# Performance work log

Measured on AMD Instinct MI355X. Metric: run time of the kernel, lower is better.

Reference implementation:

```python
import jax, jax.numpy as jnp
import numpy as np

N_NODES = 50000
N_EDGES = 800000
IN_DIM = 128
HID_DIM = 128
OUT_DIM = 64


def setup_inputs() -> dict:
    key = jax.random.key(0)
    ks = jax.random.split(key, 6)
    x = jax.random.normal(ks[0], (N_NODES, IN_DIM), dtype=jnp.float32)
    row = jax.random.randint(ks[1], (N_EDGES,), 0, N_NODES, dtype=jnp.int32)
    col = jax.random.randint(ks[2], (N_EDGES,), 0, N_NODES, dtype=jnp.int32)
    vals = jax.random.uniform(ks[3], (N_EDGES,), dtype=jnp.float32)
    # Xavier-uniform init as in nn.init.xavier_uniform_
    lim1 = float(np.sqrt(6.0 / (IN_DIM + HID_DIM)))
    lim2 = float(np.sqrt(6.0 / (HID_DIM + OUT_DIM)))
    W1 = jax.random.uniform(ks[4], (IN_DIM, HID_DIM), minval=-lim1, maxval=lim1, dtype=jnp.float32)
    W2 = jax.random.uniform(ks[5], (HID_DIM, OUT_DIM), minval=-lim2, maxval=lim2, dtype=jnp.float32)
    return {"x": x, "row": row, "col": col, "vals": vals, "W1": W1, "W2": W2}


def _spmm(row, col, vals, x):
    # out[i] = sum_{e: row[e]==i} vals[e] * x[col[e]]   (sparse adj @ x)
    msgs = vals[:, None] * x[col]  # [E, D] gathered edge messages
    return jax.ops.segment_sum(msgs, row, num_segments=N_NODES)


def reference(x, row, col, vals, W1, W2):
    # GCN layer 1: adj.mm(x) -> linear -> relu  (dropout = identity in eval)
    h = jax.nn.relu(_spmm(row, col, vals, x) @ W1)
    # GCN layer 2: adj.mm(h) -> linear (no activation)
    out = _spmm(row, col, vals, h) @ W2
    return out
```

## Files before the change

### kernel.cpp

```cpp
#include <hip/hip_runtime.h>
#include <stdint.h>

#define N_NODES 50000
#define N_EDGES 800000
#define IN_DIM 128
#define HID_DIM 128
#define OUT_DIM 64

#define ELL_CAP 64
#define XCD_GROUPS 8
#define ROWS_PER_XCD (N_NODES / XCD_GROUPS)
#define SCAT_BLOCKS_PER_XCD 256
#define SCAT_BLOCKS (SCAT_BLOCKS_PER_XCD * XCD_GROUPS)

#define INIT_BLOCKS 3300

typedef short bf16x8 __attribute__((ext_vector_type(8)));
typedef float f32x4  __attribute__((ext_vector_type(4)));

__device__ __forceinline__ uint32_t pack_bf16x2(float a, float b) {
    uint32_t ba = __float_as_uint(a), bb = __float_as_uint(b);
    ba = (ba + 0x7fffu + ((ba >> 16) & 1u)) >> 16;
    bb = (bb + 0x7fffu + ((bb >> 16) & 1u)) & 0xffff0000u;
    return ba | bb;
}

__device__ __forceinline__ unsigned short f2bf(float f) {
    uint32_t u = __float_as_uint(f);
    return (unsigned short)((u + 0x7fffu + ((u >> 16) & 1u)) >> 16);
}

__device__ __forceinline__ uint8_t f2fp8(float f) {
    uint32_t u = __float_as_uint(f);
    uint32_t s = (u >> 24) & 0x80u;
    uint32_t au = u & 0x7fffffffu;
    uint32_t r = au + 0x7FFFFu + ((au >> 20) & 1u);
    int e = (int)((r >> 23) & 0xffu) - 120;
    uint32_t m = (r >> 20) & 7u;
    uint32_t out;
    if (e <= 0) out = 0u;
    else if (e >= 16) out = 0x7Eu;
    else out = ((uint32_t)e << 3) | m;
    return (uint8_t)(s | out);
}

__device__ __forceinline__ uint32_t pack_edge(int col, float v) {
    uint32_t fb = __float_as_uint(v);
    fb = (fb + 0x7fffu + ((fb >> 16) & 1u)) & 0xffff0000u;
    return fb | (uint32_t)col;
}


__global__ __launch_bounds__(256) void init_all(int* __restrict__ counts,
                                                const float* __restrict__ W1,
                                                const float* __restrict__ W2,
                                                unsigned short* __restrict__ wt1,
                                                unsigned short* __restrict__ wt2,
                                                const int* __restrict__ col,
                                                const float* __restrict__ vals,
                                                uint32_t* __restrict__ epk) {
    int i = blockIdx.x * 256 + threadIdx.x;
    if (i < N_NODES) counts[i] = 0;
    int j = i - N_NODES;
    if (j >= 0 && j < 128 * 128) {
        int n = j >> 7, k = j & 127;
        wt1[j] = f2bf(W1[k * 128 + n]);
    }
    int l = j - 128 * 128;
    if (l >= 0 && l < 64 * 128) {
        int n = l >> 7, k = l & 127;
        wt2[l] = f2bf(W2[k * 64 + n]);
    }
    if (i < N_EDGES) epk[i] = pack_edge(col[i], vals[i]);
}


__global__ __launch_bounds__(256) void scatter_ell(const int* __restrict__ row,
                                                   const uint32_t* __restrict__ epk,
                                                   int* __restrict__ counts,
                                                   uint32_t* __restrict__ ell) {
    const int xcd = blockIdx.x & (XCD_GROUPS - 1);
    const int blk = blockIdx.x >> 3;
    const int rlo = xcd * ROWS_PER_XCD;
    int e = blk * 256 + threadIdx.x;
    const int stride = SCAT_BLOCKS_PER_XCD * 256;
    for (; e < N_EDGES; e += stride) {
        int r = row[e];
        if ((unsigned)(r - rlo) < (unsigned)ROWS_PER_XCD) {
            int p = atomicAdd(&counts[r], 1);
            if (p < ELL_CAP)
                ell[((size_t)r << 6) + p] = epk[e];
        }
    }
}


__global__ __launch_bounds__(256) void gemm_mfma1(const float* __restrict__ x,
                                                  const unsigned short* __restrict__ wt1,
                                                  uint8_t* __restrict__ t1f8) {
    const int tid = threadIdx.x;
    const int wid = tid >> 6, lane = tid & 63;
    const int l15 = lane & 15, lk = lane >> 4;
    const int n0 = blockIdx.y * 64;

    bf16x8 bfrag[4][4];
#pragma unroll
    for (int t = 0; t < 4; ++t) {
        const unsigned short* wp = wt1 + (size_t)(n0 + t * 16 + l15) * 128 + lk * 8;
#pragma unroll
        for (int s = 0; s < 4; ++s)
            bfrag[t][s] = *reinterpret_cast<const bf16x8*>(wp + s * 32);
    }

    for (int mt = blockIdx.x * 4 + wid; mt < 3125; mt += 784) {
        const int arow = mt * 16 + l15;
        bf16x8 afrag[4];
        const float* ap = x + (size_t)arow * 128 + lk * 8;
#pragma unroll
        for (int s = 0; s < 4; ++s) {
            float4 p0 = *reinterpret_cast<const float4*>(ap + s * 32);
            float4 p1 = *reinterpret_cast<const float4*>(ap + s * 32 + 4);
            bf16x8 f;
            f[0] = (short)f2bf(p0.x); f[1] = (short)f2bf(p0.y);
            f[2] = (short)f2bf(p0.z); f[3] = (short)f2bf(p0.w);
            f[4] = (short)f2bf(p1.x); f[5] = (short)f2bf(p1.y);
            f[6] = (short)f2bf(p1.z); f[7] = (short)f2bf(p1.w);
            afrag[s] = f;
        }

        f32x4 acc[4] = {{0.f,0.f,0.f,0.f},{0.f,0.f,0.f,0.f},{0.f,0.f,0.f,0.f},{0.f,0.f,0.f,0.f}};
#pragma unroll
        for (int s = 0; s < 4; ++s)
#pragma unroll
            for (int t = 0; t < 4; ++t)
                acc[t] = __builtin_amdgcn_mfma_f32_16x16x32_bf16(afrag[s], bfrag[t][s], acc[t], 0, 0, 0);

#pragma unroll
        for (int t = 0; t < 4; ++t)
#pragma unroll
            for (int q = 0; q < 4; ++q) {
                int r = mt * 16 + lk * 4 + q;
                t1f8[(size_t)r * 128 + n0 + t * 16 + l15] = f2fp8(acc[t][q]);
            }
    }
}


__global__ __launch_bounds__(256) void gemm_mfma2(const uint32_t* __restrict__ Apk,
                                                  const unsigned short* __restrict__ Wt,
                                                  unsigned short* __restrict__ outb) {
    const int tid = threadIdx.x;
    const int wid = tid >> 6, lane = tid & 63;
    const int l15 = lane & 15, lk = lane >> 4;

    bf16x8 bfrag[4][4];
#pragma unroll
    for (int t = 0; t < 4; ++t) {
        const unsigned short* wp = Wt + (size_t)(t * 16 + l15) * 128 + lk * 8;
#pragma unroll
        for (int s = 0; s < 4; ++s)
            bfrag[t][s] = *reinterpret_cast<const bf16x8*>(wp + s * 32);
    }

    for (int mt = blockIdx.x * 4 + wid; mt < 3125; mt += 784) {
        const int arow = mt * 16 + l15;
        bf16x8 afrag[4];
        const uint32_t* ap = Apk + (size_t)arow * 64 + lk * 4;
#pragma unroll
        for (int s = 0; s < 4; ++s)
            afrag[s] = *reinterpret_cast<const bf16x8*>(ap + s * 16);

        f32x4 acc[4] = {{0.f,0.f,0.f,0.f},{0.f,0.f,0.f,0.f},{0.f,0.f,0.f,0.f},{0.f,0.f,0.f,0.f}};
#pragma unroll
        for (int s = 0; s < 4; ++s)
#pragma unroll
            for (int t = 0; t < 4; ++t)
                acc[t] = __builtin_amdgcn_mfma_f32_16x16x32_bf16(afrag[s], bfrag[t][s], acc[t], 0, 0, 0);

#pragma unroll
        for (int t = 0; t < 4; ++t)
#pragma unroll
            for (int q = 0; q < 4; ++q) {
                int r = mt * 16 + lk * 4 + q;
                outb[(size_t)r * 64 + t * 16 + l15] = f2bf(acc[t][q]);
            }
    }
}


template<bool RELU>
__global__ __launch_bounds__(256) void spmm_fp8_128(const int* __restrict__ counts,
                                                    const uint32_t* __restrict__ ell,
                                                    const uint8_t* __restrict__ x8,
                                                    uint32_t* __restrict__ outp) {
    __shared__ float lut[256];
    {
        int b = threadIdx.x;
        uint32_t ee = (b >> 3) & 15u, mm = b & 7u;
        float f = (ee == 0) ? ldexpf((float)mm, -9) : ldexpf((float)(8 + mm), (int)ee - 10);
        lut[b] = (b & 0x80) ? -f : f;
    }
    __syncthreads();

    const int wid = threadIdx.x >> 6;
    const int lane = threadIdx.x & 63;
    const int r = blockIdx.x * 4 + wid;
    if (r >= N_NODES) return;
    const int start = r << 6;
    int cnt = counts[r]; if (cnt > ELL_CAP) cnt = ELL_CAP;
    const int end = start + cnt;
    const uint8_t* xb = x8 + lane * 2;

    float alo[4] = {0.f, 0.f, 0.f, 0.f};
    float ahi[4] = {0.f, 0.f, 0.f, 0.f};
    int e = start;
    for (; e + 7 < end; e += 8) {
        uint32_t c0 = ell[e],     c1 = ell[e + 1], c2 = ell[e + 2], c3 = ell[e + 3];
        uint32_t c4 = ell[e + 4], c5 = ell[e + 5], c6 = ell[e + 6], c7 = ell[e + 7];
        unsigned short u0 = *reinterpret_cast<const unsigned short*>(xb + (size_t)(c0 & 0xffffu) * 128);
        unsigned short u1 = *reinterpret_cast<const unsigned short*>(xb + (size_t)(c1 & 0xffffu) * 128);
        unsigned short u2 = *reinterpret_cast<const unsigned short*>(xb + (size_t)(c2 & 0xffffu) * 128);
        unsigned short u3 = *reinterpret_cast<const unsigned short*>(xb + (size_t)(c3 & 0xffffu) * 128);
        unsigned short u4 = *reinterpret_cast<const unsigned short*>(xb + (size_t)(c4 & 0xffffu) * 128);
        unsigned short u5 = *reinterpret_cast<const unsigned short*>(xb + (size_t)(c5 & 0xffffu) * 128);
        unsigned short u6 = *reinterpret_cast<const unsigned short*>(xb + (size_t)(c6 & 0xffffu) * 128);
        unsigned short u7 = *reinterpret_cast<const unsigned short*>(xb + (size_t)(c7 & 0xffffu) * 128);
        float v0 = __uint_as_float(c0 & 0xffff0000u), v1 = __uint_as_float(c1 & 0xffff0000u);
        float v2 = __uint_as_float(c2 & 0xffff0000u), v3 = __uint_as_float(c3 & 0xffff0000u);
        float v4 = __uint_as_float(c4 & 0xffff0000u), v5 = __uint_as_float(c5 & 0xffff0000u);
        float v6 = __uint_as_float(c6 & 0xffff0000u), v7 = __uint_as_float(c7 & 0xffff0000u);
        alo[0] = fmaf(v0, lut[u0 & 0xff], alo[0]); ahi[0] = fmaf(v0, lut[u0 >> 8], ahi[0]);
        alo[1] = fmaf(v1, lut[u1 & 0xff], alo[1]); ahi[1] = fmaf(v1, lut[u1 >> 8], ahi[1]);
        alo[2] = fmaf(v2, lut[u2 & 0xff], alo[2]); ahi[2] = fmaf(v2, lut[u2 >> 8], ahi[2]);
        alo[3] = fmaf(v3, lut[u3 & 0xff], alo[3]); ahi[3] = fmaf(v3, lut[u3 >> 8], ahi[3]);
        alo[0] = fmaf(v4, lut[u4 & 0xff], alo[0]); ahi[0] = fmaf(v4, lut[u4 >> 8], ahi[0]);
        alo[1] = fmaf(v5, lut[u5 & 0xff], alo[1]); ahi[1] = fmaf(v5, lut[u5 >> 8], ahi[1]);
        alo[2] = fmaf(v6, lut[u6 & 0xff], alo[2]); ahi[2] = fmaf(v6, lut[u6 >> 8], ahi[2]);
        alo[3] = fmaf(v7, lut[u7 & 0xff], alo[3]); ahi[3] = fmaf(v7, lut[u7 >> 8], ahi[3]);
    }
    if (e + 3 < end) {
        uint32_t c0 = ell[e], c1 = ell[e + 1], c2 = ell[e + 2], c3 = ell[e + 3];
        unsigned short u0 = *reinterpret_cast<const unsigned short*>(xb + (size_t)(c0 & 0xffffu) * 128);
        unsigned short u1 = *reinterpret_cast<const unsigned short*>(xb + (size_t)(c1 & 0xffffu) * 128);
        unsigned short u2 = *reinterpret_cast<const unsigned short*>(xb + (size_t)(c2 & 0xffffu) * 128);
        unsigned short u3 = *reinterpret_cast<const unsigned short*>(xb + (size_t)(c3 & 0xffffu) * 128);
        float v0 = __uint_as_float(c0 & 0xffff0000u), v1 = __uint_as_float(c1 & 0xffff0000u);
        float v2 = __uint_as_float(c2 & 0xffff0000u), v3 = __uint_as_float(c3 & 0xffff0000u);
        alo[0] = fmaf(v0, lut[u0 & 0xff], alo[0]); ahi[0] = fmaf(v0, lut[u0 >> 8], ahi[0]);
        alo[1] = fmaf(v1, lut[u1 & 0xff], alo[1]); ahi[1] = fmaf(v1, lut[u1 >> 8], ahi[1]);
        alo[2] = fmaf(v2, lut[u2 & 0xff], alo[2]); ahi[2] = fmaf(v2, lut[u2 >> 8], ahi[2]);
        alo[3] = fmaf(v3, lut[u3 & 0xff], alo[3]); ahi[3] = fmaf(v3, lut[u3 >> 8], ahi[3]);
        e += 4;
    }
    for (; e < end; ++e) {
        uint32_t c0 = ell[e];
        float v0 = __uint_as_float(c0 & 0xffff0000u);
        unsigned short u0 = *reinterpret_cast<const unsigned short*>(xb + (size_t)(c0 & 0xffffu) * 128);
        alo[0] = fmaf(v0, lut[u0 & 0xff], alo[0]); ahi[0] = fmaf(v0, lut[u0 >> 8], ahi[0]);
    }
    float rlo = (alo[0] + alo[1]) + (alo[2] + alo[3]);
    float rhi = (ahi[0] + ahi[1]) + (ahi[2] + ahi[3]);
    if (RELU) { rlo = fmaxf(rlo, 0.f); rhi = fmaxf(rhi, 0.f); }
    outp[(size_t)r * 64 + lane] = pack_bf16x2(rlo, rhi);
}


__global__ __launch_bounds__(256) void spmm_bf16_64(const int* __restrict__ counts,
                                                    const uint32_t* __restrict__ ell,
                                                    const uint32_t* __restrict__ xp,
                                                    float* __restrict__ out) {
    const int wid = threadIdx.x >> 6;
    const int lane = threadIdx.x & 63;
    const int r = blockIdx.x * 4 + wid;
    if (r >= N_NODES) return;
    const int start = r << 6;
    int cnt = counts[r]; if (cnt > ELL_CAP) cnt = ELL_CAP;
    const int end = start + cnt;
    const int j = lane & 31;
    const int half = lane >> 5;
    const uint32_t* xb = xp + j;

    float alo[4] = {0.f, 0.f, 0.f, 0.f};
    float ahi[4] = {0.f, 0.f, 0.f, 0.f};
    int e = start + half;
    for (; e + 6 < end; e += 8) {
        uint32_t c0 = ell[e], c1 = ell[e + 2], c2 = ell[e + 4], c3 = ell[e + 6];
        uint32_t u0 = xb[(size_t)(c0 & 0xffffu) * 32];
        uint32_t u1 = xb[(size_t)(c1 & 0xffffu) * 32];
        uint32_t u2 = xb[(size_t)(c2 & 0xffffu) * 32];
        uint32_t u3 = xb[(size_t)(c3 & 0xffffu) * 32];
        float v0 = __uint_as_float(c0 & 0xffff0000u), v1 = __uint_as_float(c1 & 0xffff0000u);
        float v2 = __uint_as_float(c2 & 0xffff0000u), v3 = __uint_as_float(c3 & 0xffff0000u);
        alo[0] = fmaf(v0, __uint_as_float(u0 << 16), alo[0]);
        ahi[0] = fmaf(v0, __uint_as_float(u0 & 0xffff0000u), ahi[0]);
        alo[1] = fmaf(v1, __uint_as_float(u1 << 16), alo[1]);
        ahi[1] = fmaf(v1, __uint_as_float(u1 & 0xffff0000u), ahi[1]);
        alo[2] = fmaf(v2, __uint_as_float(u2 << 16), alo[2]);
        ahi[2] = fmaf(v2, __uint_as_float(u2 & 0xffff0000u), ahi[2]);
        alo[3] = fmaf(v3, __uint_as_float(u3 << 16), alo[3]);
        ahi[3] = fmaf(v3, __uint_as_float(u3 & 0xffff0000u), ahi[3]);
    }
    for (; e < end; e += 2) {
        uint32_t c0 = ell[e];
        float v = __uint_as_float(c0 & 0xffff0000u);
        uint32_t u = xb[(size_t)(c0 & 0xffffu) * 32];
        alo[0] = fmaf(v, __uint_as_float(u << 16), alo[0]);
        ahi[0] = fmaf(v, __uint_as_float(u & 0xffff0000u), ahi[0]);
    }
    float alo_s = (alo[0] + alo[1]) + (alo[2] + alo[3]);
    float ahi_s = (ahi[0] + ahi[1]) + (ahi[2] + ahi[3]);
    alo_s += __shfl_xor(alo_s, 32);
    ahi_s += __shfl_xor(ahi_s, 32);
    if (half == 0) {
        float2 res = {alo_s, ahi_s};
        *reinterpret_cast<float2*>(out + (size_t)r * 64 + j * 2) = res;
    }
}


extern "C" void kernel_launch(void* const* d_in, const int* in_sizes, int n_in,
                              void* d_out, int out_size, void* d_ws, size_t ws_size,
                              hipStream_t stream) {
    const float* x    = (const float*)d_in[0];
    const int*   row  = (const int*)  d_in[1];
    const int*   col  = (const int*)  d_in[2];
    const float* vals = (const float*)d_in[3];
    const float* W1   = (const float*)d_in[4];
    const float* W2   = (const float*)d_in[5];
    float* out = (float*)d_out;

    char* ws = (char*)d_ws;
    auto align = [](size_t v) { return (v + 255) & ~(size_t)255; };
    int*      counts  = (int*)ws;              ws += align(sizeof(int) * N_NODES);
    uint32_t* epk     = (uint32_t*)ws;         ws += align(sizeof(uint32_t) * N_EDGES);
    uint32_t* ell     = (uint32_t*)ws;         ws += align(sizeof(uint32_t) * N_NODES * ELL_CAP);
    uint8_t*  t1f8    = (uint8_t*)ws;          ws += align(sizeof(uint8_t) * N_NODES * 128);
    uint32_t* hpk     = (uint32_t*)ws;         ws += align(sizeof(uint32_t) * N_NODES * 64);
    uint32_t* tpk     = (uint32_t*)ws;         ws += align(sizeof(uint32_t) * N_NODES * 32);
    unsigned short* wt1 = (unsigned short*)ws; ws += align(sizeof(short) * 128 * 128);
    unsigned short* wt2 = (unsigned short*)ws; ws += align(sizeof(short) * 64 * 128);

    init_all<<<INIT_BLOCKS, 256, 0, stream>>>(counts, W1, W2, wt1, wt2, col, vals, epk);

    scatter_ell<<<SCAT_BLOCKS, 256, 0, stream>>>(row, epk, counts, ell);

    gemm_mfma1<<<dim3(196, 2), 256, 0, stream>>>(x, wt1, t1f8);
    spmm_fp8_128<true><<<(N_NODES + 3) / 4, 256, 0, stream>>>(counts, ell, t1f8, hpk);

    gemm_mfma2<<<196, 256, 0, stream>>>(hpk, wt2, (unsigned short*)tpk);
    spmm_bf16_64<<<(N_NODES + 3) / 4, 256, 0, stream>>>(counts, ell, tpk, out);
}
```

Measured before the change: 126.6 us.

## Split SpMM feature matrices into column halves to shrink gather working set

The GEMMs now write their outputs as two separate half-width column panels, and each SpMM runs as two launches, one per panel. Each launch gathers from a table half the size (3.2 MB fp8 or 3.2 MB bf16), so the randomly indexed rows are more likely to stay in L2 or the last-level cache. In exchange, the ELL index stream and counts are read twice, there are two extra kernel launches, and each gathered row segment is narrower (64 or 32 bytes), which may waste cache-line bandwidth.

```diff
diff --git a/kernel.cpp b/kernel.cpp
--- a/kernel.cpp
+++ b/kernel.cpp
@@ -97,11 +97,13 @@
 
 __global__ __launch_bounds__(256) void gemm_mfma1(const float* __restrict__ x,
                                                   const unsigned short* __restrict__ wt1,
-                                                  uint8_t* __restrict__ t1f8) {
+                                                  uint8_t* __restrict__ t1a,
+                                                  uint8_t* __restrict__ t1b) {
     const int tid = threadIdx.x;
     const int wid = tid >> 6, lane = tid & 63;
     const int l15 = lane & 15, lk = lane >> 4;
     const int n0 = blockIdx.y * 64;
+    uint8_t* dst = (blockIdx.y == 0) ? t1a : t1b;
 
     bf16x8 bfrag[4][4];
 #pragma unroll
@@ -140,7 +142,7 @@
 #pragma unroll
             for (int q = 0; q < 4; ++q) {
                 int r = mt * 16 + lk * 4 + q;
-                t1f8[(size_t)r * 128 + n0 + t * 16 + l15] = f2fp8(acc[t][q]);
+                dst[(size_t)r * 64 + t * 16 + l15] = f2fp8(acc[t][q]);
             }
     }
 }
@@ -148,7 +150,8 @@
 
 __global__ __launch_bounds__(256) void gemm_mfma2(const uint32_t* __restrict__ Apk,
                                                   const unsigned short* __restrict__ Wt,
-                                                  unsigned short* __restrict__ outb) {
+                                                  unsigned short* __restrict__ t2a,
+                                                  unsigned short* __restrict__ t2b) {
     const int tid = threadIdx.x;
     const int wid = tid >> 6, lane = tid & 63;
     const int l15 = lane & 15, lk = lane >> 4;
@@ -182,17 +185,19 @@
 #pragma unroll
             for (int q = 0; q < 4; ++q) {
                 int r = mt * 16 + lk * 4 + q;
-                outb[(size_t)r * 64 + t * 16 + l15] = f2bf(acc[t][q]);
+                int d = t * 16 + l15;
+                unsigned short* dst = (d < 32) ? t2a : t2b;
+                dst[(size_t)r * 32 + (d & 31)] = f2bf(acc[t][q]);
             }
     }
 }
 
 
-template<bool RELU>
-__global__ __launch_bounds__(256) void spmm_fp8_128(const int* __restrict__ counts,
-                                                    const uint32_t* __restrict__ ell,
-                                                    const uint8_t* __restrict__ x8,
-                                                    uint32_t* __restrict__ outp) {
+__global__ __launch_bounds__(256) void spmm_half_fp8(const int* __restrict__ counts,
+                                                     const uint32_t* __restrict__ ell,
+                                                     const uint8_t* __restrict__ x8h,
+                                                     uint32_t* __restrict__ outp,
+                                                     int word_off) {
     __shared__ float lut[256];
     {
         int b = threadIdx.x;
@@ -202,73 +207,6 @@
     }
     __syncthreads();
 
-    const int wid = threadIdx.x >> 6;
-    const int lane = threadIdx.x & 63;
-    const int r = blockIdx.x * 4 + wid;
-    if (r >= N_NODES) return;
-    const int start = r << 6;
-    int cnt = counts[r]; if (cnt > ELL_CAP) cnt = ELL_CAP;
-    const int end = start + cnt;
-    const uint8_t* xb = x8 + lane * 2;
-
-    float alo[4] = {0.f, 0.f, 0.f, 0.f};
-    float ahi[4] = {0.f, 0.f, 0.f, 0.f};
-    int e = start;
-    for (; e + 7 < end; e += 8) {
-        uint32_t c0 = ell[e],     c1 = ell[e + 1], c2 = ell[e + 2], c3 = ell[e + 3];
-        uint32_t c4 = ell[e + 4], c5 = ell[e + 5], c6 = ell[e + 6], c7 = ell[e + 7];
-        unsigned short u0 = *reinterpret_cast<const unsigned short*>(xb + (size_t)(c0 & 0xffffu) * 128);
-        unsigned short u1 = *reinterpret_cast<const unsigned short*>(xb + (size_t)(c1 & 0xffffu) * 128);
-        unsigned short u2 = *reinterpret_cast<const unsigned short*>(xb + (size_t)(c2 & 0xffffu) * 128);
-        unsigned short u3 = *reinterpret_cast<const unsigned short*>(xb + (size_t)(c3 & 0xffffu) * 128);
-        unsigned short u4 = *reinterpret_cast<const unsigned short*>(xb + (size_t)(c4 & 0xffffu) * 128);
-        unsigned short u5 = *reinterpret_cast<const unsigned short*>(xb + (size_t)(c5 & 0xffffu) * 128);
-        unsigned short u6 = *reinterpret_cast<const unsigned short*>(xb + (size_t)(c6 & 0xffffu) * 128);
-        unsigned short u7 = *reinterpret_cast<const unsigned short*>(xb + (size_t)(c7 & 0xffffu) * 128);
-        float v0 = __uint_as_float(c0 & 0xffff0000u), v1 = __uint_as_float(c1 & 0xffff0000u);
-        float v2 = __uint_as_float(c2 & 0xffff0000u), v3 = __uint_as_float(c3 & 0xffff0000u);
-        float v4 = __uint_as_float(c4 & 0xffff0000u), v5 = __uint_as_float(c5 & 0xffff0000u);
-        float v6 = __uint_as_float(c6 & 0xffff0000u), v7 = __uint_as_float(c7 & 0xffff0000u);
-        alo[0] = fmaf(v0, lut[u0 & 0xff], alo[0]); ahi[0] = fmaf(v0, lut[u0 >> 8], ahi[0]);
-        alo[1] = fmaf(v1, lut[u1 & 0xff], alo[1]); ahi[1] = fmaf(v1, lut[u1 >> 8], ahi[1]);
-        alo[2] = fmaf(v2, lut[u2 & 0xff], alo[2]); ahi[2] = fmaf(v2, lut[u2 >> 8], ahi[2]);
-        alo[3] = fmaf(v3, lut[u3 & 0xff], alo[3]); ahi[3] = fmaf(v3, lut[u3 >> 8], ahi[3]);
-        alo[0] = fmaf(v4, lut[u4 & 0xff], alo[0]); ahi[0] = fmaf(v4, lut[u4 >> 8], ahi[0]);
-        alo[1] = fmaf(v5, lut[u5 & 0xff], alo[1]); ahi[1] = fmaf(v5, lut[u5 >> 8], ahi[1]);
-        alo[2] = fmaf(v6, lut[u6 & 0xff], alo[2]); ahi[2] = fmaf(v6, lut[u6 >> 8], ahi[2]);
-        alo[3] = fmaf(v7, lut[u7 & 0xff], alo[3]); ahi[3] = fmaf(v7, lut[u7 >> 8], ahi[3]);
-    }
-    if (e + 3 < end) {
-        uint32_t c0 = ell[e], c1 = ell[e + 1], c2 = ell[e + 2], c3 = ell[e + 3];
-        unsigned short u0 = *reinterpret_cast<const unsigned short*>(xb + (size_t)(c0 & 0xffffu) * 128);
-        unsigned short u1 = *reinterpret_cast<const unsigned short*>(xb + (size_t)(c1 & 0xffffu) * 128);
-        unsigned short u2 = *reinterpret_cast<const unsigned short*>(xb + (size_t)(c2 & 0xffffu) * 128);
-        unsigned short u3 = *reinterpret_cast<const unsigned short*>(xb + (size_t)(c3 & 0xffffu) * 128);
-        float v0 = __uint_as_float(c0 & 0xffff0000u), v1 = __uint_as_float(c1 & 0xffff0000u);
-        float v2 = __uint_as_float(c2 & 0xffff0000u), v3 = __uint_as_float(c3 & 0xffff0000u);
-        alo[0] = fmaf(v0, lut[u0 & 0xff], alo[0]); ahi[0] = fmaf(v0, lut[u0 >> 8], ahi[0]);
-        alo[1] = fmaf(v1, lut[u1 & 0xff], alo[1]); ahi[1] = fmaf(v1, lut[u1 >> 8], ahi[1]);
-        alo[2] = fmaf(v2, lut[u2 & 0xff], alo[2]); ahi[2] = fmaf(v2, lut[u2 >> 8], ahi[2]);
-        alo[3] = fmaf(v3, lut[u3 & 0xff], alo[3]); ahi[3] = fmaf(v3, lut[u3 >> 8], ahi[3]);
-        e += 4;
-    }
-    for (; e < end; ++e) {
-        uint32_t c0 = ell[e];
-        float v0 = __uint_as_float(c0 & 0xffff0000u);
-        unsigned short u0 = *reinterpret_cast<const unsigned short*>(xb + (size_t)(c0 & 0xffffu) * 128);
-        alo[0] = fmaf(v0, lut[u0 & 0xff], alo[0]); ahi[0] = fmaf(v0, lut[u0 >> 8], ahi[0]);
-    }
-    float rlo = (alo[0] + alo[1]) + (alo[2] + alo[3]);
-    float rhi = (ahi[0] + ahi[1]) + (ahi[2] + ahi[3]);
-    if (RELU) { rlo = fmaxf(rlo, 0.f); rhi = fmaxf(rhi, 0.f); }
-    outp[(size_t)r * 64 + lane] = pack_bf16x2(rlo, rhi);
-}
-
-
-__global__ __launch_bounds__(256) void spmm_bf16_64(const int* __restrict__ counts,
-                                                    const uint32_t* __restrict__ ell,
-                                                    const uint32_t* __restrict__ xp,
-                                                    float* __restrict__ out) {
     const int wid = threadIdx.x >> 6;
     const int lane = threadIdx.x & 63;
     const int r = blockIdx.x * 4 + wid;
@@ -278,17 +216,67 @@
     const int end = start + cnt;
     const int j = lane & 31;
     const int half = lane >> 5;
-    const uint32_t* xb = xp + j;
+    const uint8_t* xb = x8h + j * 2;
 
     float alo[4] = {0.f, 0.f, 0.f, 0.f};
     float ahi[4] = {0.f, 0.f, 0.f, 0.f};
     int e = start + half;
     for (; e + 6 < end; e += 8) {
         uint32_t c0 = ell[e], c1 = ell[e + 2], c2 = ell[e + 4], c3 = ell[e + 6];
-        uint32_t u0 = xb[(size_t)(c0 & 0xffffu) * 32];
-        uint32_t u1 = xb[(size_t)(c1 & 0xffffu) * 32];
-        uint32_t u2 = xb[(size_t)(c2 & 0xffffu) * 32];
-        uint32_t u3 = xb[(size_t)(c3 & 0xffffu) * 32];
+        unsigned short u0 = *reinterpret_cast<const unsigned short*>(xb + (size_t)(c0 & 0xffffu) * 64);
+        unsigned short u1 = *reinterpret_cast<const unsigned short*>(xb + (size_t)(c1 & 0xffffu) * 64);
+        unsigned short u2 = *reinterpret_cast<const unsigned short*>(xb + (size_t)(c2 & 0xffffu) * 64);
+        unsigned short u3 = *reinterpret_cast<const unsigned short*>(xb + (size_t)(c3 & 0xffffu) * 64);
+        float v0 = __uint_as_float(c0 & 0xffff0000u), v1 = __uint_as_float(c1 & 0xffff0000u);
+        float v2 = __uint_as_float(c2 & 0xffff0000u), v3 = __uint_as_float(c3 & 0xffff0000u);
+        alo[0] = fmaf(v0, lut[u0 & 0xff], alo[0]); ahi[0] = fmaf(v0, lut[u0 >> 8], ahi[0]);
+        alo[1] = fmaf(v1, lut[u1 & 0xff], alo[1]); ahi[1] = fmaf(v1, lut[u1 >> 8], ahi[1]);
+        alo[2] = fmaf(v2, lut[u2 & 0xff], alo[2]); ahi[2] = fmaf(v2, lut[u2 >> 8], ahi[2]);
+        alo[3] = fmaf(v3, lut[u3 & 0xff], alo[3]); ahi[3] = fmaf(v3, lut[u3 >> 8], ahi[3]);
+    }
+    for (; e < end; e += 2) {
+        uint32_t c0 = ell[e];
+        float v = __uint_as_float(c0 & 0xffff0000u);
+        unsigned short u = *reinterpret_cast<const unsigned short*>(xb + (size_t)(c0 & 0xffffu) * 64);
+        alo[0] = fmaf(v, lut[u & 0xff], alo[0]); ahi[0] = fmaf(v, lut[u >> 8], ahi[0]);
+    }
+    float rlo = (alo[0] + alo[1]) + (alo[2] + alo[3]);
+    float rhi = (ahi[0] + ahi[1]) + (ahi[2] + ahi[3]);
+    rlo += __shfl_xor(rlo, 32);
+    rhi += __shfl_xor(rhi, 32);
+    if (half == 0) {
+        rlo = fmaxf(rlo, 0.f);
+        rhi = fmaxf(rhi, 0.f);
+        outp[(size_t)r * 64 + word_off + j] = pack_bf16x2(rlo, rhi);
+    }
+}
+
+
+__global__ __launch_bounds__(256) void spmm_half_bf16(const int* __restrict__ counts,
+                                                      const uint32_t* __restrict__ ell,
+                                                      const uint32_t* __restrict__ xph,
+                                                      float* __restrict__ out,
+                                                      int dim_off) {
+    const int wid = threadIdx.x >> 6;
+    const int lane = threadIdx.x & 63;
+    const int r = blockIdx.x * 4 + wid;
+    if (r >= N_NODES) return;
+    const int start = r << 6;
+    int cnt = counts[r]; if (cnt > ELL_CAP) cnt = ELL_CAP;
+    const int end = start + cnt;
+    const int j = lane & 15;
+    const int g = lane >> 4;
+    const uint32_t* xb = xph + j;
+
+    float alo[4] = {0.f, 0.f, 0.f, 0.f};
+    float ahi[4] = {0.f, 0.f, 0.f, 0.f};
+    int e = start + g;
+    for (; e + 12 < end; e += 16) {
+        uint32_t c0 = ell[e], c1 = ell[e + 4], c2 = ell[e + 8], c3 = ell[e + 12];
+        uint32_t u0 = xb[(size_t)(c0 & 0xffffu) * 16];
+        uint32_t u1 = xb[(size_t)(c1 & 0xffffu) * 16];
+        uint32_t u2 = xb[(size_t)(c2 & 0xffffu) * 16];
+        uint32_t u3 = xb[(size_t)(c3 & 0xffffu) * 16];
         float v0 = __uint_as_float(c0 & 0xffff0000u), v1 = __uint_as_float(c1 & 0xffff0000u);
         float v2 = __uint_as_float(c2 & 0xffff0000u), v3 = __uint_as_float(c3 & 0xffff0000u);
         alo[0] = fmaf(v0, __uint_as_float(u0 << 16), alo[0]);
@@ -300,20 +288,22 @@
         alo[3] = fmaf(v3, __uint_as_float(u3 << 16), alo[3]);
         ahi[3] = fmaf(v3, __uint_as_float(u3 & 0xffff0000u), ahi[3]);
     }
-    for (; e < end; e += 2) {
+    for (; e < end; e += 4) {
         uint32_t c0 = ell[e];
         float v = __uint_as_float(c0 & 0xffff0000u);
-        uint32_t u = xb[(size_t)(c0 & 0xffffu) * 32];
+        uint32_t u = xb[(size_t)(c0 & 0xffffu) * 16];
         alo[0] = fmaf(v, __uint_as_float(u << 16), alo[0]);
         ahi[0] = fmaf(v, __uint_as_float(u & 0xffff0000u), ahi[0]);
     }
     float alo_s = (alo[0] + alo[1]) + (alo[2] + alo[3]);
     float ahi_s = (ahi[0] + ahi[1]) + (ahi[2] + ahi[3]);
+    alo_s += __shfl_xor(alo_s, 16);
+    ahi_s += __shfl_xor(ahi_s, 16);
     alo_s += __shfl_xor(alo_s, 32);
     ahi_s += __shfl_xor(ahi_s, 32);
-    if (half == 0) {
+    if (lane < 16) {
         float2 res = {alo_s, ahi_s};
-        *reinterpret_cast<float2*>(out + (size_t)r * 64 + j * 2) = res;
+        *reinterpret_cast<float2*>(out + (size_t)r * 64 + dim_off + j * 2) = res;
     }
 }
 
@@ -334,9 +324,11 @@
     int*      counts  = (int*)ws;              ws += align(sizeof(int) * N_NODES);
     uint32_t* epk     = (uint32_t*)ws;         ws += align(sizeof(uint32_t) * N_EDGES);
     uint32_t* ell     = (uint32_t*)ws;         ws += align(sizeof(uint32_t) * N_NODES * ELL_CAP);
-    uint8_t*  t1f8    = (uint8_t*)ws;          ws += align(sizeof(uint8_t) * N_NODES * 128);
+    uint8_t*  t1a     = (uint8_t*)ws;          ws += align(sizeof(uint8_t) * N_NODES * 64);
+    uint8_t*  t1b     = (uint8_t*)ws;          ws += align(sizeof(uint8_t) * N_NODES * 64);
     uint32_t* hpk     = (uint32_t*)ws;         ws += align(sizeof(uint32_t) * N_NODES * 64);
-    uint32_t* tpk     = (uint32_t*)ws;         ws += align(sizeof(uint32_t) * N_NODES * 32);
+    unsigned short* t2a = (unsigned short*)ws; ws += align(sizeof(short) * N_NODES * 32);
+    unsigned short* t2b = (unsigned short*)ws; ws += align(sizeof(short) * N_NODES * 32);
     unsigned short* wt1 = (unsigned short*)ws; ws += align(sizeof(short) * 128 * 128);
     unsigned short* wt2 = (unsigned short*)ws; ws += align(sizeof(short) * 64 * 128);
 
@@ -344,9 +336,11 @@
 
     scatter_ell<<<SCAT_BLOCKS, 256, 0, stream>>>(row, epk, counts, ell);
 
-    gemm_mfma1<<<dim3(196, 2), 256, 0, stream>>>(x, wt1, t1f8);
-    spmm_fp8_128<true><<<(N_NODES + 3) / 4, 256, 0, stream>>>(counts, ell, t1f8, hpk);
-
-    gemm_mfma2<<<196, 256, 0, stream>>>(hpk, wt2, (unsigned short*)tpk);
-    spmm_bf16_64<<<(N_NODES + 3) / 4, 256, 0, stream>>>(counts, ell, tpk, out);
-}
+    gemm_mfma1<<<dim3(196, 2), 256, 0, stream>>>(x, wt1, t1a, t1b);
+    spmm_half_fp8<<<(N_NODES + 3) / 4, 256, 0, stream>>>(counts, ell, t1a, hpk, 0);
+    spmm_half_fp8<<<(N_NODES + 3) / 4, 256, 0, stream>>>(counts, ell, t1b, hpk, 32);
+
+    gemm_mfma2<<<196, 256, 0, stream>>>(hpk, wt2, t2a, t2b);
+    spmm_half_bf16<<<(N_NODES + 3) / 4, 256, 0, stream>>>(counts, ell, (const uint32_t*)t2a, out, 0);
+    spmm_half_bf16<<<(N_NODES + 3) / 4, 256, 0, stream>>>(counts, ell, (const uint32_t*)t2b, out, 32);
+}
```

New measurement: 160.8 us. 27.0% more time.
